# Kernel optimization log

Measured on AMD Instinct MI355X. Metric: run time of the kernel, lower is better.

The kernel has to match this reference:

```python
import jax, jax.numpy as jnp
import numpy as np

TEMPERATURE = 0.6
TOP_K = 50
TOP_P = 0.9
REP_PENALTY = 1.2
BATCH, VOCAB, HIST = 256, 128000, 200


def setup_inputs() -> dict:
    key = jax.random.key(0)
    k1, k2 = jax.random.split(key)
    logits = jax.random.normal(k1, (BATCH, VOCAB), dtype=jnp.float32)
    prev_tokens = jax.random.randint(k2, (BATCH, HIST), 0, VOCAB)
    return {"logits": logits, "prev_tokens": prev_tokens}


def reference(logits, prev_tokens):
    B = logits.shape[0]
    rows = jnp.arange(B)[:, None]  # [B,1] row index for scatter

    # --- repetition penalty: mult if <0 else div, on previously seen tokens ---
    vals = jnp.take_along_axis(logits, prev_tokens, axis=1)  # [B,H]
    penalized = jnp.where(vals < 0, vals * REP_PENALTY, vals / REP_PENALTY)
    logits = logits.at[rows, prev_tokens].set(penalized)

    # --- temperature ---
    logits = logits / TEMPERATURE

    # --- top-k filter: mask everything below the k-th largest logit ---
    kth = jax.lax.top_k(logits, TOP_K)[0][:, -1:]  # [B,1]
    logits = jnp.where(logits < kth, -jnp.inf, logits)

    # --- top-p (nucleus) filter: sort desc, cumsum probs, keep prefix <= p ---
    order = jnp.argsort(-logits, axis=-1)                      # [B,V] desc order
    sorted_logits = jnp.take_along_axis(logits, order, axis=-1)
    cum_probs = jnp.cumsum(jax.nn.softmax(sorted_logits, axis=-1), axis=-1)
    remove_sorted = cum_probs > TOP_P
    # shift right so the first token exceeding p is kept (HF semantics)
    remove_sorted = jnp.concatenate(
        [jnp.zeros_like(remove_sorted[:, :1]), remove_sorted[:, :-1]], axis=-1)
    # scatter mask back to vocab order
    remove = jnp.zeros_like(remove_sorted).at[rows, order].set(remove_sorted)
    logits = jnp.where(remove, -jnp.inf, logits)

    # --- distribution parameter of Multinomial(total_count=compare_sample) ---
    probs = jax.nn.softmax(logits, axis=-1)
    return probs
```

## Files before the change

### kernel.cpp

```cpp
#include <hip/hip_runtime.h>
#include <stdint.h>

#define BATCH    256
#define VOCAB    128000
#define HIST     200
#define TOPK     50
#define CAP      2048
#define NTHREADS 1024
#define BITWORDS (VOCAB / 32)


__device__ __forceinline__ unsigned fkey_of(float f) {
  unsigned u = __float_as_uint(f);
  return (u & 0x80000000u) ? ~u : (u | 0x80000000u);
}
__device__ __forceinline__ float f_of_key(unsigned k) {
  unsigned u = (k & 0x80000000u) ? (k & 0x7FFFFFFFu) : ~k;
  return __uint_as_float(u);
}

__global__ __launch_bounds__(NTHREADS) void sample_head_kernel(
    const float* __restrict__ logits, const int* __restrict__ prev,
    float* __restrict__ out)
{
  __shared__ unsigned bitmask[BITWORDS];
  __shared__ unsigned long long keys[CAP];
  __shared__ unsigned long long skeys[CAP];
  __shared__ float evals[CAP];
  __shared__ int s_count;
  __shared__ int s_m, s_j;
  __shared__ float s_maxx, s_Z2;

  const int b   = blockIdx.x;
  const int tid = threadIdx.x;
  const float* row  = logits + (size_t)b * VOCAB;
  float*       orow = out    + (size_t)b * VOCAB;

  for (int i = tid; i < BITWORDS; i += NTHREADS) bitmask[i] = 0u;
  if (tid == 0) s_count = 0;
  __syncthreads();
  for (int i = tid; i < HIST; i += NTHREADS) {
    int t = prev[b * HIST + i];
    atomicOr(&bitmask[t >> 5], 1u << (t & 31));
  }
  __syncthreads();

  const float4* row4  = (const float4*)row;
  float4*       orow4 = (float4*)orow;
  const int N4 = VOCAB / 4;

  float T = 3.0f;

  for (int i = tid; i < N4; i += NTHREADS) {
    float4 v4 = row4[i];
    orow4[i] = make_float4(0.f, 0.f, 0.f, 0.f);
    int v0 = i * 4;
    unsigned w  = bitmask[v0 >> 5];
    unsigned sh = v0 & 31;
    float vv[4] = {v4.x, v4.y, v4.z, v4.w};
    #pragma unroll
    for (int l = 0; l < 4; ++l) {
      float v = vv[l];
      float y = v;
      if ((w >> (sh + l)) & 1u)
        y = (v < 0.0f) ? v * 1.2f : v / 1.2f;
      if (y > T) {
        float x = y / 0.6f;
        int pos = atomicAdd(&s_count, 1);
        if (pos < CAP) {
          unsigned k = fkey_of(x);
          keys[pos] = ((unsigned long long)k << 32) |
                      (unsigned)(~(unsigned)(v0 + l));
        }
      }
    }
  }
  __syncthreads();
  int cnt = s_count;

  if (cnt < TOPK || cnt > CAP) {
    float Tlo = 0.f, Thi = 0.f;
    bool hasLo = false, hasHi = false;
    for (int attempt = 0; attempt < 40; ++attempt) {
      if (cnt < TOPK) { Thi = T; hasHi = true; T = hasLo ? 0.5f * (T + Tlo) : T - 1.0f; }
      else            { Tlo = T; hasLo = true; T = hasHi ? 0.5f * (T + Thi) : T + 1.0f; }
      __syncthreads();
      if (tid == 0) s_count = 0;
      __syncthreads();
      for (int i = tid; i < N4; i += NTHREADS) {
        float4 v4 = row4[i];
        int v0 = i * 4;
        unsigned w  = bitmask[v0 >> 5];
        unsigned sh = v0 & 31;
        float vv[4] = {v4.x, v4.y, v4.z, v4.w};
        #pragma unroll
        for (int l = 0; l < 4; ++l) {
          float v = vv[l];
          float y = v;
          if ((w >> (sh + l)) & 1u)
            y = (v < 0.0f) ? v * 1.2f : v / 1.2f;
          if (y > T) {
            float x = y / 0.6f;
            int pos = atomicAdd(&s_count, 1);
            if (pos < CAP) {
              unsigned k = fkey_of(x);
              keys[pos] = ((unsigned long long)k << 32) |
                          (unsigned)(~(unsigned)(v0 + l));
            }
          }
        }
      }
      __syncthreads();
      cnt = s_count;
      if (cnt >= TOPK && cnt <= CAP) break;
    }
    if (cnt > CAP) cnt = CAP;
  }

  for (int i = tid; i < cnt; i += NTHREADS) {
    unsigned long long a = keys[i];
    int r = 0;
    for (int j = 0; j < cnt; ++j) r += (keys[j] > a);
    skeys[r] = a;
  }
  __syncthreads();

  if (tid == 0) {
    int kk = (cnt < TOPK) ? cnt : TOPK;
    unsigned kth = (unsigned)(skeys[kk - 1] >> 32);
    int m = kk;
    while (m < cnt && (unsigned)(skeys[m] >> 32) == kth) m++;
    s_m = m;
    s_maxx = f_of_key((unsigned)(skeys[0] >> 32));
  }
  __syncthreads();
  int m = s_m;
  float maxx = s_maxx;
  for (int i = tid; i < m; i += NTHREADS)
    evals[i] = expf(f_of_key((unsigned)(skeys[i] >> 32)) - maxx);
  __syncthreads();

  if (tid == 0) {
    float Z = 0.f;
    for (int i = 0; i < m; ++i) Z += evals[i];
    float cum = 0.f;
    int j = 0;
    for (int i = 0; i < m; ++i) {
      if (i > 0 && cum > 0.9f) break;
      cum += evals[i] / Z;
      j = i + 1;
    }
    float Z2 = 0.f;
    for (int i = 0; i < j; ++i) Z2 += evals[i];
    s_j = j; s_Z2 = Z2;
  }
  __syncthreads();

  int j = s_j;
  float Z2 = s_Z2;
  for (int i = tid; i < j; i += NTHREADS) {
    int idx = (int)(~(unsigned)(skeys[i] & 0xFFFFFFFFull));
    orow[idx] = evals[i] / Z2;
  }
}

extern "C" void kernel_launch(void* const* d_in, const int* in_sizes, int n_in,
                              void* d_out, int out_size, void* d_ws, size_t ws_size,
                              hipStream_t stream) {
  const float* logits = (const float*)d_in[0];
  const int*   prev   = (const int*)d_in[1];
  float*       out    = (float*)d_out;
  hipLaunchKernelGGL(sample_head_kernel, dim3(BATCH), dim3(NTHREADS), 0, stream,
                     logits, prev, out);
}
```

Baseline: 241.9 us.

## Batch four vector loads and zero-stores per thread with inline asm

The main scan is restructured so each thread issues four 16-byte global loads and four zero-stores at once through inline assembly. It then waits only for the loads, leaving the stores in flight, so more memory traffic is outstanding per thread in a single-block-per-row kernel. A cheap max-of-four prefilter skips the bitmask lookup and per-element penalty work for vectors that cannot exceed the threshold. This is valid because the penalty never increases a value. A scalar tail loop covers the remainder, and the hand-written wait counts depend on the GPU's in-order vector memory counter semantics.

```diff
diff --git a/kernel.cpp b/kernel.cpp
--- a/kernel.cpp
+++ b/kernel.cpp
@@ -8,7 +8,11 @@
 #define CAP      2048
 #define NTHREADS 1024
 #define BITWORDS (VOCAB / 32)
-
+#define N4       (VOCAB / 4)
+#define MAIN4    28672
+
+
+typedef float f32x4_t __attribute__((ext_vector_type(4)));
 
 __device__ __forceinline__ unsigned fkey_of(float f) {
   unsigned u = __float_as_uint(f);
@@ -17,6 +21,9 @@
 __device__ __forceinline__ float f_of_key(unsigned k) {
   unsigned u = (k & 0x80000000u) ? (k & 0x7FFFFFFFu) : ~k;
   return __uint_as_float(u);
+}
+__device__ __forceinline__ float max4v(f32x4_t v) {
+  return fmaxf(fmaxf(v[0], v[1]), fmaxf(v[2], v[3]));
 }
 
 __global__ __launch_bounds__(NTHREADS) void sample_head_kernel(
@@ -45,36 +52,92 @@
   }
   __syncthreads();
 
-  const float4* row4  = (const float4*)row;
-  float4*       orow4 = (float4*)orow;
-  const int N4 = VOCAB / 4;
+  const f32x4_t* rowx = (const f32x4_t*)row;
+  f32x4_t*       outx = (f32x4_t*)orow;
 
   float T = 3.0f;
 
-  for (int i = tid; i < N4; i += NTHREADS) {
-    float4 v4 = row4[i];
-    orow4[i] = make_float4(0.f, 0.f, 0.f, 0.f);
-    int v0 = i * 4;
-    unsigned w  = bitmask[v0 >> 5];
-    unsigned sh = v0 & 31;
-    float vv[4] = {v4.x, v4.y, v4.z, v4.w};
+  const f32x4_t z4q = (f32x4_t)0.f;
+  for (int it = 0; it < 7; ++it) {
+    const int j0 = it * 4096 + tid;
+    const f32x4_t* p0 = rowx + j0;
+    const f32x4_t* p1 = p0 + 1024;
+    const f32x4_t* p2 = p0 + 2048;
+    const f32x4_t* p3 = p0 + 3072;
+    f32x4_t* q0 = outx + j0;
+    f32x4_t* q1 = q0 + 1024;
+    f32x4_t* q2 = q0 + 2048;
+    f32x4_t* q3 = q0 + 3072;
+    f32x4_t a, bb, c, d;
+    asm volatile(
+        "global_load_dwordx4 %0, %4, off\n\t"
+        "global_load_dwordx4 %1, %5, off\n\t"
+        "global_load_dwordx4 %2, %6, off\n\t"
+        "global_load_dwordx4 %3, %7, off\n\t"
+        "global_store_dwordx4 %8, %12, off\n\t"
+        "global_store_dwordx4 %9, %12, off\n\t"
+        "global_store_dwordx4 %10, %12, off\n\t"
+        "global_store_dwordx4 %11, %12, off\n\t"
+        "s_waitcnt vmcnt(4)"
+        : "=&v"(a), "=&v"(bb), "=&v"(c), "=&v"(d)
+        : "v"(p0), "v"(p1), "v"(p2), "v"(p3),
+          "v"(q0), "v"(q1), "v"(q2), "v"(q3), "v"(z4q)
+        : "memory");
+
+    f32x4_t vv[4] = {a, bb, c, d};
     #pragma unroll
-    for (int l = 0; l < 4; ++l) {
-      float v = vv[l];
-      float y = v;
-      if ((w >> (sh + l)) & 1u)
-        y = (v < 0.0f) ? v * 1.2f : v / 1.2f;
-      if (y > T) {
-        float x = y / 0.6f;
-        int pos = atomicAdd(&s_count, 1);
-        if (pos < CAP) {
-          unsigned k = fkey_of(x);
-          keys[pos] = ((unsigned long long)k << 32) |
-                      (unsigned)(~(unsigned)(v0 + l));
+    for (int g = 0; g < 4; ++g) {
+      const int j = j0 + g * 1024;
+      const f32x4_t v = vv[g];
+      if (max4v(v) > T) {
+        unsigned e0 = 4u * (unsigned)j;
+        unsigned w  = bitmask[e0 >> 5];
+        unsigned sh = e0 & 31;
+        #pragma unroll
+        for (int l = 0; l < 4; ++l) {
+          float vl = v[l];
+          float y = vl;
+          if ((w >> (sh + l)) & 1u)
+            y = (vl < 0.0f) ? vl * 1.2f : vl / 1.2f;
+          if (y > T) {
+            float x = y / 0.6f;
+            int pos = atomicAdd(&s_count, 1);
+            if (pos < CAP) {
+              unsigned k = fkey_of(x);
+              keys[pos] = ((unsigned long long)k << 32) |
+                          (unsigned)(~(unsigned)(e0 + l));
+            }
+          }
         }
       }
     }
   }
+  for (int i = MAIN4 + tid; i < N4; i += NTHREADS) {
+    f32x4_t v = rowx[i];
+    outx[i] = z4q;
+    if (max4v(v) > T) {
+      unsigned e0 = 4u * (unsigned)i;
+      unsigned w  = bitmask[e0 >> 5];
+      unsigned sh = e0 & 31;
+      #pragma unroll
+      for (int l = 0; l < 4; ++l) {
+        float vl = v[l];
+        float y = vl;
+        if ((w >> (sh + l)) & 1u)
+          y = (vl < 0.0f) ? vl * 1.2f : vl / 1.2f;
+        if (y > T) {
+          float x = y / 0.6f;
+          int pos = atomicAdd(&s_count, 1);
+          if (pos < CAP) {
+            unsigned k = fkey_of(x);
+            keys[pos] = ((unsigned long long)k << 32) |
+                        (unsigned)(~(unsigned)(e0 + l));
+          }
+        }
+      }
+    }
+  }
+  asm volatile("s_waitcnt vmcnt(0)" ::: "memory");
   __syncthreads();
   int cnt = s_count;
 
@@ -88,14 +151,13 @@
       if (tid == 0) s_count = 0;
       __syncthreads();
       for (int i = tid; i < N4; i += NTHREADS) {
-        float4 v4 = row4[i];
+        f32x4_t v4 = rowx[i];
         int v0 = i * 4;
         unsigned w  = bitmask[v0 >> 5];
         unsigned sh = v0 & 31;
-        float vv[4] = {v4.x, v4.y, v4.z, v4.w};
         #pragma unroll
         for (int l = 0; l < 4; ++l) {
-          float v = vv[l];
+          float v = v4[l];
           float y = v;
           if ((w >> (sh + l)) & 1u)
             y = (v < 0.0f) ? v * 1.2f : v / 1.2f;
```

New measurement: 242.6 us. About the same (+0.3%).
